# Optimization experiments

Measured on AMD Instinct MI355X. Metric: run time of the kernel, lower is better.

The kernel has to match this reference:

```python
import jax, jax.numpy as jnp
import numpy as np

N_NODES, N_EDGES, FEA_DIM, H_DIM, N_LAYER, N_GRAPHS, LABEL_DIM = 50000, 600000, 128, 256, 3, 256, 2


def setup_inputs() -> dict:
    key = jax.random.key(0)
    ks = jax.random.split(key, 8)
    x = jax.random.normal(ks[0], (N_NODES, FEA_DIM), jnp.float32)
    edge_index = jax.random.randint(ks[1], (2, N_EDGES), 0, N_NODES, dtype=jnp.int64)
    batch = jnp.sort(jax.random.randint(ks[2], (N_NODES,), 0, N_GRAPHS, dtype=jnp.int64))
    Wg = jax.random.normal(ks[3], (N_LAYER, FEA_DIM, FEA_DIM), jnp.float32) / np.sqrt(FEA_DIM)
    bg = jnp.zeros((N_LAYER, FEA_DIM), jnp.float32)
    w1 = jax.random.normal(ks[4], (FEA_DIM, H_DIM), jnp.float32) / np.sqrt(FEA_DIM)
    b1 = jnp.zeros((H_DIM,), jnp.float32)
    w2 = jax.random.normal(ks[5], (H_DIM, LABEL_DIM), jnp.float32) / np.sqrt(H_DIM)
    b2 = jnp.zeros((LABEL_DIM,), jnp.float32)
    return dict(x=x, Wg=Wg, bg=bg, w1=w1, b1=b1, w2=w2, b2=b2,
                edge_index=edge_index, batch=batch)


def reference(x, Wg, bg, w1, b1, w2, b2, edge_index, batch):
    N = x.shape[0]
    # --- GCN normalization with self-loops (PyG GCNConv default) ---
    loop = jnp.arange(N, dtype=edge_index.dtype)
    src = jnp.concatenate([edge_index[0], loop])  # [E+N]
    dst = jnp.concatenate([edge_index[1], loop])
    deg = jax.ops.segment_sum(jnp.ones_like(src, x.dtype), dst, num_segments=N)
    dinv = jnp.where(deg > 0, jax.lax.rsqrt(jnp.maximum(deg, 1.0)), 0.0)
    norm = dinv[src] * dinv[dst]  # [E+N]
    # --- stacked GCNConv + ReLU ---
    for l in range(Wg.shape[0]):
        h = x @ Wg[l]                              # [N, D] linear transform
        msg = h[src] * norm[:, None]               # gather + edge scale
        x = jax.ops.segment_sum(msg, dst, num_segments=N) + bg[l]  # scatter-add
        x = jax.nn.relu(x)
    # --- global mean pool over graphs ---
    sums = jax.ops.segment_sum(x, batch, num_segments=N_GRAPHS)
    counts = jax.ops.segment_sum(jnp.ones((N, 1), x.dtype), batch, num_segments=N_GRAPHS)
    pooled = sums / jnp.maximum(counts, 1.0)       # [G, D]
    # --- MLP head ---
    h = jax.nn.relu(pooled @ w1 + b1)
    return h @ w2 + b2                             # [G, label_dim]
```

## Files before the change

kernel.cpp:

```cpp
#include <hip/hip_runtime.h>
#include <hip/hip_bf16.h>

#define N_NODES 50000
#define N_EDGES 600000
#define FEA_DIM 128
#define H_DIM 256
#define N_LAYER 3
#define N_GRAPHS 256
#define LABEL_DIM 2

#define SCAN_NB ((N_NODES + 255) / 256)


__global__ __launch_bounds__(256) void k_count(const int* __restrict__ dst, int* __restrict__ counts) {
    int e = blockIdx.x * 256 + threadIdx.x;
    if (e < N_EDGES) atomicAdd(&counts[dst[e]], 1);
}

__global__ __launch_bounds__(256) void k_partial(const int* __restrict__ counts, int* __restrict__ partial) {
    int g = blockIdx.x * 256 + threadIdx.x;
    int v = (g < N_NODES) ? counts[g] : 0;
#pragma unroll
    for (int off = 32; off > 0; off >>= 1) v += __shfl_down(v, off);
    __shared__ int ws[4];
    int lane = threadIdx.x & 63, wid = threadIdx.x >> 6;
    if (lane == 0) ws[wid] = v;
    __syncthreads();
    if (threadIdx.x == 0) partial[blockIdx.x] = ws[0] + ws[1] + ws[2] + ws[3];
}

__global__ __launch_bounds__(256) void k_rowptr(const int* __restrict__ counts, const int* __restrict__ partial,
                                                int* __restrict__ row_ptr, float* __restrict__ dinv) {
    __shared__ int sp[256];
    __shared__ int s[256];
    int tid = threadIdx.x;
    sp[tid] = (tid < SCAN_NB) ? partial[tid] : 0;
    __syncthreads();
#pragma unroll
    for (int off = 1; off < 256; off <<= 1) {
        int t = (tid >= off) ? sp[tid - off] : 0;
        __syncthreads();
        sp[tid] += t;
        __syncthreads();
    }
    int block_off = (blockIdx.x == 0) ? 0 : sp[blockIdx.x - 1];

    int g = blockIdx.x * 256 + tid;
    int c = (g < N_NODES) ? counts[g] : 0;
    s[tid] = c;
    __syncthreads();
#pragma unroll
    for (int off = 1; off < 256; off <<= 1) {
        int t = (tid >= off) ? s[tid - off] : 0;
        __syncthreads();
        s[tid] += t;
        __syncthreads();
    }
    if (g < N_NODES) {
        row_ptr[g] = block_off + s[tid] - c;
        dinv[g] = rsqrtf((float)c + 1.0f);
    }
    if (blockIdx.x == 0 && tid == 0) row_ptr[N_NODES] = sp[SCAN_NB - 1];
}

__global__ __launch_bounds__(256) void k_fill(const int* __restrict__ src, const int* __restrict__ dst,
                                              const int* __restrict__ row_ptr, int* __restrict__ cursor,
                                              int* __restrict__ col) {
    int e = blockIdx.x * 256 + threadIdx.x;
    if (e >= N_EDGES) return;
    int s = src[e], d = dst[e];
    int p = row_ptr[d] + atomicAdd(&cursor[d], 1);
    col[p] = s;
}


__global__ __launch_bounds__(256) void k_gemm(const float* __restrict__ X, const float* __restrict__ W,
                                              float* __restrict__ H, int M) {
    __shared__ float a_s[32][132];
    __shared__ float b_s[32][128];
    const int tid = threadIdx.x;
    const int row_g = tid >> 4;
    const int col_g = tid & 15;
    const int row_base = blockIdx.x * 128;
    float acc[8][8] = {};

    for (int kt = 0; kt < 4; ++kt) {
        const int k0 = kt * 32;
#pragma unroll
        for (int j = 0; j < 4; ++j) {
            int id = tid + j * 256;
            int m = id >> 3;
            int kq = (id & 7) << 2;
            float4 v = make_float4(0.f, 0.f, 0.f, 0.f);
            int gr = row_base + m;
            if (gr < M) v = *(const float4*)(X + gr * 128 + k0 + kq);
            a_s[kq + 0][m] = v.x; a_s[kq + 1][m] = v.y;
            a_s[kq + 2][m] = v.z; a_s[kq + 3][m] = v.w;
        }
#pragma unroll
        for (int j = 0; j < 4; ++j) {
            int id = tid + j * 256;
            int k = id >> 5;
            int n = (id & 31) << 2;
            *(float4*)(&b_s[k][n]) = *(const float4*)(W + (k0 + k) * 128 + n);
        }
        __syncthreads();
#pragma unroll 8
        for (int k = 0; k < 32; ++k) {
            float4 a0 = *(const float4*)(&a_s[k][row_g * 8]);
            float4 a1 = *(const float4*)(&a_s[k][row_g * 8 + 4]);
            float4 b0 = *(const float4*)(&b_s[k][col_g * 4]);
            float4 b1 = *(const float4*)(&b_s[k][64 + col_g * 4]);
            float av[8] = {a0.x, a0.y, a0.z, a0.w, a1.x, a1.y, a1.z, a1.w};
            float bv[8] = {b0.x, b0.y, b0.z, b0.w, b1.x, b1.y, b1.z, b1.w};
#pragma unroll
            for (int i = 0; i < 8; ++i)
#pragma unroll
                for (int jj = 0; jj < 8; ++jj) acc[i][jj] += av[i] * bv[jj];
        }
        __syncthreads();
    }
#pragma unroll
    for (int i = 0; i < 8; ++i) {
        int gr = row_base + row_g * 8 + i;
        if (gr < M) {
            float4 o0 = {acc[i][0], acc[i][1], acc[i][2], acc[i][3]};
            float4 o1 = {acc[i][4], acc[i][5], acc[i][6], acc[i][7]};
            *(float4*)(H + gr * 128 + col_g * 4) = o0;
            *(float4*)(H + gr * 128 + 64 + col_g * 4) = o1;
        }
    }
}


__global__ __launch_bounds__(256) void k_agg(const float* __restrict__ H, const float* __restrict__ bgl,
                                             const int* __restrict__ row_ptr, const int* __restrict__ col,
                                             const float* __restrict__ dinv,
                                             float* __restrict__ Xo) {
    int wave = (blockIdx.x * 256 + threadIdx.x) >> 6;
    int lane = threadIdx.x & 63;
    if (wave >= N_NODES) return;
    const int i = wave;
    const float2* H2 = (const float2*)H;
    const float di = dinv[i];
    float2 h = H2[i * 64 + lane];
    float2 acc;
    acc.x = h.x * di * di;
    acc.y = h.y * di * di;
    const int p0 = row_ptr[i], p1 = row_ptr[i + 1];
    for (int base = p0; base < p1; base += 64) {
        int m = p1 - base; if (m > 64) m = 64;
        int sc = 0; float wc = 0.f;
        if (lane < m) { sc = col[base + lane]; wc = dinv[sc] * di; }
        for (int j = 0; j < m; j += 8) {
            int cnt = m - j; if (cnt > 8) cnt = 8;
            float2 hbuf[8]; float wbuf[8];
#pragma unroll
            for (int t = 0; t < 8; ++t) {
                if (t < cnt) {
                    int s = __shfl(sc, j + t);
                    wbuf[t] = __shfl(wc, j + t);
                    hbuf[t] = H2[s * 64 + lane];
                }
            }
#pragma unroll
            for (int t = 0; t < 8; ++t) {
                if (t < cnt) {
                    acc.x += hbuf[t].x * wbuf[t];
                    acc.y += hbuf[t].y * wbuf[t];
                }
            }
        }
    }
    float2 b = ((const float2*)bgl)[lane];
    float2 o;
    o.x = fmaxf(acc.x + b.x, 0.f);
    o.y = fmaxf(acc.y + b.y, 0.f);
    ((float2*)Xo)[i * 64 + lane] = o;
}


__global__ __launch_bounds__(256) void k_poolmlp(const float* __restrict__ X, const int* __restrict__ batch,
                                                 const float* __restrict__ w1, const float* __restrict__ b1,
                                                 const float* __restrict__ w2, const float* __restrict__ b2,
                                                 float* __restrict__ out) {
    __shared__ int s_lo, s_hi;
    __shared__ float red[256];
    __shared__ float xs[128];
    __shared__ float hs[256];
    int g = blockIdx.x, tid = threadIdx.x;
    if (tid == 0) {
        int lo = 0, hi = N_NODES;
        while (lo < hi) { int mid = (lo + hi) >> 1; if (batch[mid] < g) lo = mid + 1; else hi = mid; }
        s_lo = lo;
        int lo2 = lo, hi2 = N_NODES;
        while (lo2 < hi2) { int mid = (lo2 + hi2) >> 1; if (batch[mid] < g + 1) lo2 = mid + 1; else hi2 = mid; }
        s_hi = lo2;
    }
    __syncthreads();
    int lo = s_lo, hi = s_hi;
    int f = tid & 127, half = tid >> 7;
    float acc = 0.f;
    for (int r = lo + half; r < hi; r += 2) acc += X[r * 128 + f];
    red[tid] = acc;
    __syncthreads();
    if (tid < 128) {
        int cnt = hi - lo;
        xs[tid] = (red[tid] + red[tid + 128]) / (float)(cnt > 0 ? cnt : 1);
    }
    __syncthreads();
    float a1 = b1[tid];
#pragma unroll 8
    for (int k = 0; k < 128; ++k) a1 += xs[k] * w1[k * H_DIM + tid];
    hs[tid] = fmaxf(a1, 0.f);
    __syncthreads();
    int j = tid >> 7, t2 = tid & 127;
    float p = hs[t2] * w2[t2 * LABEL_DIM + j] + hs[t2 + 128] * w2[(t2 + 128) * LABEL_DIM + j];
    red[tid] = p;
    __syncthreads();
    for (int s2 = 64; s2 > 0; s2 >>= 1) {
        if (t2 < s2) red[tid] += red[tid + s2];
        __syncthreads();
    }
    if (t2 == 0) out[g * LABEL_DIM + j] = red[tid] + b2[j];
}


extern "C" void kernel_launch(void* const* d_in, const int* in_sizes, int n_in,
                              void* d_out, int out_size, void* d_ws, size_t ws_size,
                              hipStream_t stream) {
    const float* x   = (const float*)d_in[0];
    const float* Wg  = (const float*)d_in[1];
    const float* bg  = (const float*)d_in[2];
    const float* w1  = (const float*)d_in[3];
    const float* b1  = (const float*)d_in[4];
    const float* w2  = (const float*)d_in[5];
    const float* b2  = (const float*)d_in[6];
    const int* eidx  = (const int*)d_in[7];
    const int* batch = (const int*)d_in[8];
    float* out = (float*)d_out;

    const int* src = eidx;
    const int* dst = eidx + N_EDGES;

    char* ws = (char*)d_ws;
    size_t off = 0;
    float* A = (float*)(ws + off); off += (size_t)N_NODES * FEA_DIM * 4;
    float* B = (float*)(ws + off); off += (size_t)N_NODES * FEA_DIM * 4;
    int*   col = (int*)(ws + off); off += (size_t)N_EDGES * 4;
    int*   row_ptr = (int*)(ws + off); off += 200704;
    int*   cursor  = (int*)(ws + off); off += 200704;
    int*   counts  = (int*)(ws + off); off += 200704;
    float* dinv    = (float*)(ws + off); off += 200704;
    int*   partial = (int*)(ws + off); off += 4096;

    hipMemsetAsync(cursor, 0, 2 * 200704, stream);
    k_count<<<(N_EDGES + 255) / 256, 256, 0, stream>>>(dst, counts);
    k_partial<<<SCAN_NB, 256, 0, stream>>>(counts, partial);
    k_rowptr<<<SCAN_NB, 256, 0, stream>>>(counts, partial, row_ptr, dinv);
    k_fill<<<(N_EDGES + 255) / 256, 256, 0, stream>>>(src, dst, row_ptr, cursor, col);

    const float* cur = x;
    for (int l = 0; l < N_LAYER; ++l) {
        k_gemm<<<(N_NODES + 127) / 128, 256, 0, stream>>>(cur, Wg + (size_t)l * FEA_DIM * FEA_DIM, B, N_NODES);
        k_agg<<<(N_NODES + 3) / 4, 256, 0, stream>>>(B, bg + (size_t)l * FEA_DIM, row_ptr, col, dinv, A);
        cur = A;
    }
    k_poolmlp<<<N_GRAPHS, 256, 0, stream>>>(A, batch, w1, b1, w2, b2, out);
}
```

Measured before the change: 422.5 us.

## Fuse first-layer GEMM with CSR fill and shrink GEMM tile to 64 rows

Merges the CSR column-fill kernel with the layer-0 GEMM in a single launch. The first GEMM_NB blocks compute X·W0 and the remaining blocks scatter edges into the CSR, so the two independent jobs share the GPU. The cursor reset moves into the row-pointer kernel, so the memset only clears counts. The GEMM tile shrinks from 128 to 64 rows per block, giving more blocks and fewer accumulators per thread, at the cost of reloading W tiles more often. Aggregation indices are widened to size_t.

```diff
diff --git a/kernel.cpp b/kernel.cpp
--- a/kernel.cpp
+++ b/kernel.cpp
@@ -10,6 +10,8 @@
 #define LABEL_DIM 2
 
 #define SCAN_NB ((N_NODES + 255) / 256)
+#define GEMM_NB ((N_NODES + 63) / 64)
+#define EDGE_NB ((N_EDGES + 255) / 256)
 
 
 __global__ __launch_bounds__(256) void k_count(const int* __restrict__ dst, int* __restrict__ counts) {
@@ -17,77 +19,21 @@
     if (e < N_EDGES) atomicAdd(&counts[dst[e]], 1);
 }
 
-__global__ __launch_bounds__(256) void k_partial(const int* __restrict__ counts, int* __restrict__ partial) {
-    int g = blockIdx.x * 256 + threadIdx.x;
-    int v = (g < N_NODES) ? counts[g] : 0;
-#pragma unroll
-    for (int off = 32; off > 0; off >>= 1) v += __shfl_down(v, off);
-    __shared__ int ws[4];
-    int lane = threadIdx.x & 63, wid = threadIdx.x >> 6;
-    if (lane == 0) ws[wid] = v;
-    __syncthreads();
-    if (threadIdx.x == 0) partial[blockIdx.x] = ws[0] + ws[1] + ws[2] + ws[3];
-}
-
-__global__ __launch_bounds__(256) void k_rowptr(const int* __restrict__ counts, const int* __restrict__ partial,
-                                                int* __restrict__ row_ptr, float* __restrict__ dinv) {
-    __shared__ int sp[256];
-    __shared__ int s[256];
-    int tid = threadIdx.x;
-    sp[tid] = (tid < SCAN_NB) ? partial[tid] : 0;
-    __syncthreads();
-#pragma unroll
-    for (int off = 1; off < 256; off <<= 1) {
-        int t = (tid >= off) ? sp[tid - off] : 0;
-        __syncthreads();
-        sp[tid] += t;
-        __syncthreads();
-    }
-    int block_off = (blockIdx.x == 0) ? 0 : sp[blockIdx.x - 1];
-
-    int g = blockIdx.x * 256 + tid;
-    int c = (g < N_NODES) ? counts[g] : 0;
-    s[tid] = c;
-    __syncthreads();
-#pragma unroll
-    for (int off = 1; off < 256; off <<= 1) {
-        int t = (tid >= off) ? s[tid - off] : 0;
-        __syncthreads();
-        s[tid] += t;
-        __syncthreads();
-    }
-    if (g < N_NODES) {
-        row_ptr[g] = block_off + s[tid] - c;
-        dinv[g] = rsqrtf((float)c + 1.0f);
-    }
-    if (blockIdx.x == 0 && tid == 0) row_ptr[N_NODES] = sp[SCAN_NB - 1];
-}
-
-__global__ __launch_bounds__(256) void k_fill(const int* __restrict__ src, const int* __restrict__ dst,
-                                              const int* __restrict__ row_ptr, int* __restrict__ cursor,
-                                              int* __restrict__ col) {
-    int e = blockIdx.x * 256 + threadIdx.x;
-    if (e >= N_EDGES) return;
-    int s = src[e], d = dst[e];
-    int p = row_ptr[d] + atomicAdd(&cursor[d], 1);
-    col[p] = s;
-}
-
-
-__global__ __launch_bounds__(256) void k_gemm(const float* __restrict__ X, const float* __restrict__ W,
-                                              float* __restrict__ H, int M) {
-    __shared__ float a_s[32][132];
+
+__device__ __forceinline__ void gemm_body(const float* __restrict__ X, const float* __restrict__ W,
+                                          float* __restrict__ H, int M, int tile) {
+    __shared__ float a_s[32][68];
     __shared__ float b_s[32][128];
     const int tid = threadIdx.x;
     const int row_g = tid >> 4;
     const int col_g = tid & 15;
-    const int row_base = blockIdx.x * 128;
-    float acc[8][8] = {};
+    const int row_base = tile * 64;
+    float acc[4][8] = {};
 
     for (int kt = 0; kt < 4; ++kt) {
         const int k0 = kt * 32;
 #pragma unroll
-        for (int j = 0; j < 4; ++j) {
+        for (int j = 0; j < 2; ++j) {
             int id = tid + j * 256;
             int m = id >> 3;
             int kq = (id & 7) << 2;
@@ -107,22 +53,21 @@
         __syncthreads();
 #pragma unroll 8
         for (int k = 0; k < 32; ++k) {
-            float4 a0 = *(const float4*)(&a_s[k][row_g * 8]);
-            float4 a1 = *(const float4*)(&a_s[k][row_g * 8 + 4]);
+            float4 a0 = *(const float4*)(&a_s[k][row_g * 4]);
             float4 b0 = *(const float4*)(&b_s[k][col_g * 4]);
             float4 b1 = *(const float4*)(&b_s[k][64 + col_g * 4]);
-            float av[8] = {a0.x, a0.y, a0.z, a0.w, a1.x, a1.y, a1.z, a1.w};
+            float av[4] = {a0.x, a0.y, a0.z, a0.w};
             float bv[8] = {b0.x, b0.y, b0.z, b0.w, b1.x, b1.y, b1.z, b1.w};
 #pragma unroll
-            for (int i = 0; i < 8; ++i)
+            for (int i = 0; i < 4; ++i)
 #pragma unroll
                 for (int jj = 0; jj < 8; ++jj) acc[i][jj] += av[i] * bv[jj];
         }
         __syncthreads();
     }
 #pragma unroll
-    for (int i = 0; i < 8; ++i) {
-        int gr = row_base + row_g * 8 + i;
+    for (int i = 0; i < 4; ++i) {
+        int gr = row_base + row_g * 4 + i;
         if (gr < M) {
             float4 o0 = {acc[i][0], acc[i][1], acc[i][2], acc[i][3]};
             float4 o1 = {acc[i][4], acc[i][5], acc[i][6], acc[i][7]};
@@ -130,6 +75,77 @@
             *(float4*)(H + gr * 128 + 64 + col_g * 4) = o1;
         }
     }
+}
+
+__global__ __launch_bounds__(256) void k_gemm(const float* __restrict__ X, const float* __restrict__ W,
+                                              float* __restrict__ H, int M) {
+    gemm_body(X, W, H, M, blockIdx.x);
+}
+
+__global__ __launch_bounds__(256) void k_gemm0_fill(const float* __restrict__ X, const float* __restrict__ W,
+                                                    float* __restrict__ H,
+                                                    const int* __restrict__ src, const int* __restrict__ dst,
+                                                    const int* __restrict__ row_ptr, int* __restrict__ cursor,
+                                                    int* __restrict__ col) {
+    if (blockIdx.x < GEMM_NB) {
+        gemm_body(X, W, H, N_NODES, blockIdx.x);
+    } else {
+        int e = (blockIdx.x - GEMM_NB) * 256 + threadIdx.x;
+        if (e < N_EDGES) {
+            int s = src[e], d = dst[e];
+            int p = row_ptr[d] + atomicAdd(&cursor[d], 1);
+            col[p] = s;
+        }
+    }
+}
+
+
+__global__ __launch_bounds__(256) void k_partial(const int* __restrict__ counts, int* __restrict__ partial) {
+    int g = blockIdx.x * 256 + threadIdx.x;
+    int v = (g < N_NODES) ? counts[g] : 0;
+#pragma unroll
+    for (int off = 32; off > 0; off >>= 1) v += __shfl_down(v, off);
+    __shared__ int ws[4];
+    int lane = threadIdx.x & 63, wid = threadIdx.x >> 6;
+    if (lane == 0) ws[wid] = v;
+    __syncthreads();
+    if (threadIdx.x == 0) partial[blockIdx.x] = ws[0] + ws[1] + ws[2] + ws[3];
+}
+
+__global__ __launch_bounds__(256) void k_rowptr(const int* __restrict__ counts, const int* __restrict__ partial,
+                                                int* __restrict__ row_ptr, float* __restrict__ dinv,
+                                                int* __restrict__ cursor) {
+    __shared__ int sp[256];
+    __shared__ int s[256];
+    int tid = threadIdx.x;
+    sp[tid] = (tid < SCAN_NB) ? partial[tid] : 0;
+    __syncthreads();
+#pragma unroll
+    for (int off = 1; off < 256; off <<= 1) {
+        int t = (tid >= off) ? sp[tid - off] : 0;
+        __syncthreads();
+        sp[tid] += t;
+        __syncthreads();
+    }
+    int block_off = (blockIdx.x == 0) ? 0 : sp[blockIdx.x - 1];
+
+    int g = blockIdx.x * 256 + tid;
+    int c = (g < N_NODES) ? counts[g] : 0;
+    s[tid] = c;
+    __syncthreads();
+#pragma unroll
+    for (int off = 1; off < 256; off <<= 1) {
+        int t = (tid >= off) ? s[tid - off] : 0;
+        __syncthreads();
+        s[tid] += t;
+        __syncthreads();
+    }
+    if (g < N_NODES) {
+        row_ptr[g] = block_off + s[tid] - c;
+        dinv[g] = rsqrtf((float)c + 1.0f);
+        cursor[g] = 0;
+    }
+    if (blockIdx.x == 0 && tid == 0) row_ptr[N_NODES] = sp[SCAN_NB - 1];
 }
 
 
@@ -143,7 +159,7 @@
     const int i = wave;
     const float2* H2 = (const float2*)H;
     const float di = dinv[i];
-    float2 h = H2[i * 64 + lane];
+    float2 h = H2[(size_t)i * 64 + lane];
     float2 acc;
     acc.x = h.x * di * di;
     acc.y = h.y * di * di;
@@ -160,7 +176,7 @@
                 if (t < cnt) {
                     int s = __shfl(sc, j + t);
                     wbuf[t] = __shfl(wc, j + t);
-                    hbuf[t] = H2[s * 64 + lane];
+                    hbuf[t] = H2[(size_t)s * 64 + lane];
                 }
             }
 #pragma unroll
@@ -176,7 +192,7 @@
     float2 o;
     o.x = fmaxf(acc.x + b.x, 0.f);
     o.y = fmaxf(acc.y + b.y, 0.f);
-    ((float2*)Xo)[i * 64 + lane] = o;
+    ((float2*)Xo)[(size_t)i * 64 + lane] = o;
 }
 
 
@@ -254,17 +270,16 @@
     float* dinv    = (float*)(ws + off); off += 200704;
     int*   partial = (int*)(ws + off); off += 4096;
 
-    hipMemsetAsync(cursor, 0, 2 * 200704, stream);
-    k_count<<<(N_EDGES + 255) / 256, 256, 0, stream>>>(dst, counts);
+    hipMemsetAsync(counts, 0, 200704, stream);
+    k_count<<<EDGE_NB, 256, 0, stream>>>(dst, counts);
     k_partial<<<SCAN_NB, 256, 0, stream>>>(counts, partial);
-    k_rowptr<<<SCAN_NB, 256, 0, stream>>>(counts, partial, row_ptr, dinv);
-    k_fill<<<(N_EDGES + 255) / 256, 256, 0, stream>>>(src, dst, row_ptr, cursor, col);
-
-    const float* cur = x;
-    for (int l = 0; l < N_LAYER; ++l) {
-        k_gemm<<<(N_NODES + 127) / 128, 256, 0, stream>>>(cur, Wg + (size_t)l * FEA_DIM * FEA_DIM, B, N_NODES);
+    k_rowptr<<<SCAN_NB, 256, 0, stream>>>(counts, partial, row_ptr, dinv, cursor);
+    k_gemm0_fill<<<GEMM_NB + EDGE_NB, 256, 0, stream>>>(x, Wg, B, src, dst, row_ptr, cursor, col);
+
+    k_agg<<<(N_NODES + 3) / 4, 256, 0, stream>>>(B, bg + 0 * FEA_DIM, row_ptr, col, dinv, A);
+    for (int l = 1; l < N_LAYER; ++l) {
+        k_gemm<<<GEMM_NB, 256, 0, stream>>>(A, Wg + (size_t)l * FEA_DIM * FEA_DIM, B, N_NODES);
         k_agg<<<(N_NODES + 3) / 4, 256, 0, stream>>>(B, bg + (size_t)l * FEA_DIM, row_ptr, col, dinv, A);
-        cur = A;
     }
     k_poolmlp<<<N_GRAPHS, 256, 0, stream>>>(A, batch, w1, b1, w2, b2, out);
 }
```

Measured after the change: 387.4 us. 8.3% less time.
